# Performance work log

Hardware: AMD Instinct MI355X
Metric: run time of the kernel (lower is better)

Reference implementation:

```python
import jax, jax.numpy as jnp
import numpy as np

# Module hyperparameters (from init_kwargs)
CH = 512        # channels
H = 8           # num_heads
D = CH // H     # head_dim = 64
K = 64          # max_kernel_size
HALF_S = 16     # max_samples // 2
S = 2 * HALF_S + 1  # 33 sample taps
MAX_F = 16.0
MIN_F = 1.0
MAX_RECEPTIVE = HALF_S * MAX_F  # 256.0


def setup_inputs() -> dict:
    key = jax.random.key(0)
    ks = jax.random.split(key, 5)
    B, L = 2, 2048
    x = jax.random.normal(ks[0], (B, L, CH), dtype=jnp.float32)
    wave_w = jax.random.normal(ks[1], (2 * H, CH), dtype=jnp.float32) * 0.02
    wave_b = jnp.zeros((2 * H,), dtype=jnp.float32)
    kernel_w = jax.random.normal(ks[2], (H * K, CH), dtype=jnp.float32) * 0.02
    kernel_b = jnp.zeros((H * K,), dtype=jnp.float32)
    out_w = jax.random.normal(ks[3], (CH, CH), dtype=jnp.float32) * 0.02
    return {"x": x, "wave_w": wave_w, "wave_b": wave_b,
            "kernel_w": kernel_w, "kernel_b": kernel_b, "out_w": out_w}


def _silu(v):
    return v * jax.nn.sigmoid(v)


def _gather_conv(x, freq, phase, kernel):
    """Learned-frequency gather convolution.
    x:      [B,L,C]      freq,phase: [B,L,H]      kernel: [B,L,H,K]
    For each query position t and head h, sample S positions
      pos_j = t + phase + (j - half_s) * freq,   j = 0..S-1
    clamped to a receptive window of +-max_receptive around t and to [0,L-1],
    gathered with linear interpolation, weighted by per-position kernel taps.
    Phase receives no gradient (torch backward returns d_phase=None).
    """
    B, L, C = x.shape
    xh = x.reshape(B, L, H, D).transpose(0, 2, 1, 3)  # [B,H,L,D]
    t = jnp.arange(L, dtype=x.dtype)                  # [L]
    offs = jnp.arange(S, dtype=x.dtype) - HALF_S      # [S]
    phase_sg = jax.lax.stop_gradient(phase)
    tb = t[None, :, None, None]
    pos = tb + phase_sg[..., None] + offs * freq[..., None]   # [B,L,H,S]
    pos = jnp.clip(pos, tb - MAX_RECEPTIVE, tb + MAX_RECEPTIVE)
    pos = jnp.clip(pos, 0.0, L - 1)
    p0 = jnp.floor(pos)
    w = (pos - p0).transpose(0, 2, 1, 3)[..., None]           # [B,H,L,S,1]
    i0 = p0.astype(jnp.int32).transpose(0, 2, 1, 3).reshape(B, H, L * S)
    i1 = jnp.minimum(i0 + 1, L - 1)
    g0 = jnp.take_along_axis(xh, i0[..., None], axis=2).reshape(B, H, L, S, D)
    g1 = jnp.take_along_axis(xh, i1[..., None], axis=2).reshape(B, H, L, S, D)
    g = (1.0 - w) * g0 + w * g1                               # [B,H,L,S,D]
    k = kernel[..., :S].transpose(0, 2, 1, 3)                 # [B,H,L,S]
    outh = jnp.einsum('bhls,bhlsd->bhld', k, g)               # [B,H,L,D]
    return outh.transpose(0, 2, 1, 3).reshape(B, L, C)


def reference(x, wave_w, wave_b, kernel_w, kernel_b, out_w):
    B, L, C = x.shape
    wave = _silu(x @ wave_w.T + wave_b).reshape(B, L, 2, H)
    freq = jax.nn.sigmoid(wave[:, :, 0, :]) * (MAX_F - MIN_F) + MIN_F  # [B,L,H]
    phase = jnp.tanh(wave[:, :, 1, :]) * MAX_F                         # [B,L,H]
    kern = _silu(x @ kernel_w.T + kernel_b).reshape(B, L, H, K)
    hidden = _gather_conv(x, freq, phase, kern)                        # [B,L,C]
    return _silu(hidden @ out_w.T)
```

## Files before the change

### kernel.cpp

```cpp
#include <hip/hip_runtime.h>
#include <cstdint>
#include <cstddef>

#define LSEQ   2048
#define CHN    512
#define NH     8
#define HD     64
#define NTAP   33
#define NPOS   4096
#define MAXREC 256.0f

typedef __bf16   bf16x8 __attribute__((ext_vector_type(8)));
typedef __bf16   bf16x4 __attribute__((ext_vector_type(4)));
typedef float    f32x4  __attribute__((ext_vector_type(4)));
typedef _Float16 f16x2  __attribute__((ext_vector_type(2)));

__device__ __forceinline__ float silu_f(float v) {
    return v / (1.0f + expf(-v));
}

__device__ __forceinline__ void gload_lds16(const void* g, void* l) {
    __builtin_amdgcn_global_load_lds((const __attribute__((address_space(1))) void*)g,
                                     (__attribute__((address_space(3))) void*)l, 16, 0, 0);
}

__device__ __forceinline__ float fdot2f(unsigned a, unsigned b, float c) {
#if __has_builtin(__builtin_amdgcn_fdot2)
    return __builtin_amdgcn_fdot2(__builtin_bit_cast(f16x2, a),
                                  __builtin_bit_cast(f16x2, b), c, false);
#else
    f16x2 av = __builtin_bit_cast(f16x2, a);
    f16x2 bv = __builtin_bit_cast(f16x2, b);
    return c + (float)av[0] * (float)bv[0] + (float)av[1] * (float)bv[1];
#endif
}


__global__ __launch_bounds__(256) void fused_prep(
    const float* __restrict__ x, const float* __restrict__ ww,
    const float* __restrict__ wb,
    const float* __restrict__ kernel_w, __bf16* __restrict__ kwb,
    const float* __restrict__ out_w,    __bf16* __restrict__ owb,
    unsigned* __restrict__ tab, __bf16* __restrict__ xb,
    unsigned* __restrict__ xpair)
{
    __shared__ float wwS[16 * 512];
    __shared__ float fphS[4][16];

    int tid = threadIdx.x;
    if (blockIdx.x < 256) {
        const float* src = (blockIdx.x < 128) ? kernel_w : out_w;
        __bf16*      dst = (blockIdx.x < 128) ? kwb : owb;
        int C = ((blockIdx.x & 127) * 256 + tid);
        int tileIdx = C / (64 * 8);
        int o    = (C % (64 * 8)) * 16;
        int rowL = o >> 7;
        int cb   = o & 127;
        int cbu  = cb ^ ((rowL & 7) << 4);
        int block = cbu >> 6;
        int g2    = (cbu >> 4) & 3;
        int rs = (tileIdx >> 3) * 64 + rowL;
        int kb = (tileIdx & 7) * 64 + block * 32 + g2 * 4;
        const float* s = src + (size_t)rs * 512 + kb;
        float4 v0 = *(const float4*)s;
        float4 v1 = *(const float4*)(s + 16);
        bf16x8 r;
        r[0] = (__bf16)v0.x; r[1] = (__bf16)v0.y; r[2] = (__bf16)v0.z; r[3] = (__bf16)v0.w;
        r[4] = (__bf16)v1.x; r[5] = (__bf16)v1.y; r[6] = (__bf16)v1.z; r[7] = (__bf16)v1.w;
        *(bf16x8*)(dst + (size_t)C * 8) = r;
        return;
    }

    #pragma unroll
    for (int j = 0; j < 8; ++j) {
        int idx = tid * 4 + j * 1024;
        *(float4*)&wwS[idx] = *(const float4*)&ww[idx];
    }

    int wid  = tid >> 6;
    int lane = tid & 63;
    int pos  = (blockIdx.x - 256) * 4 + wid;
    int t    = pos & (LSEQ - 1);

    const float* xrow = x + (size_t)pos * CHN;
    float4 xa = *(const float4*)(xrow + lane * 8);
    float4 xv = *(const float4*)(xrow + lane * 8 + 4);
    int nxt = (t == LSEQ - 1) ? pos : pos + 1;
    const float* nrow = x + (size_t)nxt * CHN;
    float4 na = *(const float4*)(nrow + lane * 8);
    float4 nv = *(const float4*)(nrow + lane * 8 + 4);
    float xs[8];
    #pragma unroll
    for (int j = 0; j < 8; ++j) xs[j] = xrow[lane + 64 * j];

    {
        int kloc = (lane * 8) & 63;
        int kt   = lane >> 3;
        int rowL = pos & 63;
        int blk  = kloc >> 5;
        int kkA  = kloc & 31;
        int kkV  = kkA + 4;
        int colA = blk * 32 + 8 * ((kkA & 15) >> 2) + 4 * ((kkA >> 4) & 1);
        int colV = blk * 32 + 8 * ((kkV & 15) >> 2) + 4 * ((kkV >> 4) & 1);
        int sw   = (rowL & 7) << 4;
        char* base = (char*)xb + (((size_t)(pos >> 6) * 8 + kt) * 8192) + rowL * 128;
        bf16x4 va = { (__bf16)xa.x, (__bf16)xa.y, (__bf16)xa.z, (__bf16)xa.w };
        bf16x4 vv = { (__bf16)xv.x, (__bf16)xv.y, (__bf16)xv.z, (__bf16)xv.w };
        *(bf16x4*)(base + ((colA * 2) ^ sw)) = va;
        *(bf16x4*)(base + ((colV * 2) ^ sw)) = vv;
    }

    {
        float va8[8] = {xa.x, xa.y, xa.z, xa.w, xv.x, xv.y, xv.z, xv.w};
        float nb8[8] = {na.x, na.y, na.z, na.w, nv.x, nv.y, nv.z, nv.w};
        unsigned u[8];
        #pragma unroll
        for (int j = 0; j < 8; ++j) {
            unsigned short lo = __builtin_bit_cast(unsigned short, (_Float16)va8[j]);
            unsigned short hi = __builtin_bit_cast(unsigned short, (_Float16)nb8[j]);
            u[j] = (unsigned)lo | ((unsigned)hi << 16);
        }
        unsigned* dp = xpair + (size_t)pos * 512 + lane * 8;
        *(uint4*)dp       = make_uint4(u[0], u[1], u[2], u[3]);
        *(uint4*)(dp + 4) = make_uint4(u[4], u[5], u[6], u[7]);
    }

    __syncthreads();

    #pragma unroll
    for (int o = 0; o < 16; ++o) {
        const float* wr = &wwS[o * 512 + lane];
        float p = 0.0f;
        #pragma unroll
        for (int j = 0; j < 8; ++j) p = fmaf(xs[j], wr[64 * j], p);
        #pragma unroll
        for (int off = 32; off > 0; off >>= 1) p += __shfl_xor(p, off);
        if (lane == 0) {
            float v = p + wb[o];
            float s = silu_f(v);
            fphS[wid][o] = (o < 8) ? (1.0f + 15.0f / (1.0f + expf(-s)))
                                   : (tanhf(s) * 16.0f);
        }
    }
    __syncthreads();

    float tf = (float)t;
    float lo = fmaxf(tf - MAXREC, 0.0f);
    float hi = fminf(tf + MAXREC, (float)(LSEQ - 1));
    for (int it = lane; it < NH * NTAP; it += 64) {
        int h = it & 7, s = it >> 3;
        float f  = fphS[wid][h];
        float ph = fphS[wid][8 + h];
        float p = (tf + ph) + (float)(s - 16) * f;
        p = fminf(fmaxf(p, lo), hi);
        float p0 = floorf(p);
        float w  = p - p0;
        int i0 = (int)p0;
        if (i0 >= LSEQ - 1) { i0 = LSEQ - 2; w = 1.0f; }
        _Float16 hw = (_Float16)w;
        unsigned u = ((unsigned)i0 << 16) |
                     (unsigned)__builtin_bit_cast(unsigned short, hw);
        tab[(size_t)pos * (NH * NTAP) + it] = u;
    }
}

template<bool COMPACT>
__global__ __launch_bounds__(256) void gemm_mfma64(
    const __bf16* __restrict__ At, const __bf16* __restrict__ Bt,
    const float* __restrict__ bias, float* __restrict__ C,
    uint2* __restrict__ qtab, const unsigned* __restrict__ tab)
{
    __shared__ __bf16 As[2][64 * 64];
    __shared__ __bf16 Bs[2][64 * 64];

    int bm = blockIdx.x, bn = blockIdx.y;
    int tid  = threadIdx.x;
    int lane = tid & 63;
    int wid  = tid >> 6;
    int wr = wid >> 1, wc = wid & 1;
    int lg = lane >> 4, l15 = lane & 15;

    const __bf16* Abase = At + (size_t)bm * 8 * 4096;
    const __bf16* Bbase = Bt + (size_t)bn * 8 * 4096;

    int offA[2][2], offB[2][2];
    #pragma unroll
    for (int mi = 0; mi < 2; ++mi) {
        int row = wr * 32 + mi * 16 + l15;
        #pragma unroll
        for (int ks = 0; ks < 2; ++ks)
            offA[mi][ks] = row * 128 + (((ks << 6) | (lg << 4)) ^ ((row & 7) << 4));
    }
    #pragma unroll
    for (int ni = 0; ni < 2; ++ni) {
        int n = wc * 32 + ni * 16 + l15;
        #pragma unroll
        for (int ks = 0; ks < 2; ++ks)
            offB[ni][ks] = n * 128 + (((ks << 6) | (lg << 4)) ^ ((n & 7) << 4));
    }

    f32x4 acc[2][2] = {};

    auto stage = [&](int b, int kt) {
        const __bf16* ga = Abase + (size_t)kt * 4096 + tid * 8;
        const __bf16* gb = Bbase + (size_t)kt * 4096 + tid * 8;
        __bf16* la = &As[b][tid * 8];
        __bf16* lb = &Bs[b][tid * 8];
        #pragma unroll
        for (int c = 0; c < 2; ++c) gload_lds16(ga + c * 2048, la + c * 2048);
        #pragma unroll
        for (int c = 0; c < 2; ++c) gload_lds16(gb + c * 2048, lb + c * 2048);
    };

    stage(0, 0);
    #pragma unroll
    for (int kt = 0; kt < 8; ++kt) {
        int cur = kt & 1;
        if (kt < 7) stage(cur ^ 1, kt + 1);
        __builtin_amdgcn_sched_barrier(0);
        if (kt < 7) asm volatile("s_waitcnt vmcnt(4)" ::: "memory");
        else        asm volatile("s_waitcnt vmcnt(0)" ::: "memory");
        __builtin_amdgcn_s_barrier();
        const char* ab = (const char*)&As[cur][0];
        const char* bb = (const char*)&Bs[cur][0];
        #pragma unroll
        for (int ks = 0; ks < 2; ++ks) {
            bf16x8 af[2], bfr[2];
            #pragma unroll
            for (int mi = 0; mi < 2; ++mi) af[mi]  = *(const bf16x8*)(ab + offA[mi][ks]);
            #pragma unroll
            for (int ni = 0; ni < 2; ++ni) bfr[ni] = *(const bf16x8*)(bb + offB[ni][ks]);
            #pragma unroll
            for (int mi = 0; mi < 2; ++mi)
                #pragma unroll
                for (int ni = 0; ni < 2; ++ni)
                    acc[mi][ni] = __builtin_amdgcn_mfma_f32_16x16x32_bf16(
                        af[mi], bfr[ni], acc[mi][ni], 0, 0, 0);
        }
        __builtin_amdgcn_s_barrier();
    }

    int n0 = bn * 64 + wc * 32 + l15;
    #pragma unroll
    for (int ni = 0; ni < 2; ++ni) {
        int n = n0 + ni * 16;
        float bv = bias ? bias[n] : 0.0f;
        #pragma unroll
        for (int mi = 0; mi < 2; ++mi) {
            int m = bm * 64 + wr * 32 + mi * 16 + lg * 4;
            #pragma unroll
            for (int j = 0; j < 4; ++j) {
                float v = silu_f(acc[mi][ni][j] + bv);
                if (COMPACT) {
                    int h = n >> 6, sc = n & 63;
                    if (sc < NTAP) {
                        unsigned u = tab[(size_t)(m + j) * (NH * NTAP) + sc * 8 + h];
                        float w = (float)__builtin_bit_cast(
                            _Float16, (unsigned short)(u & 0xFFFFu));
                        float t1 = v * w;
                        unsigned short c0 =
                            __builtin_bit_cast(unsigned short, (_Float16)(v - t1));
                        unsigned short c1 =
                            __builtin_bit_cast(unsigned short, (_Float16)t1);
                        uint2 qv;
                        qv.x = (unsigned)c0 | ((unsigned)c1 << 16);
                        qv.y = (u >> 16) << 11;
                        qtab[(size_t)(m + j) * (NTAP * 8) + sc * 8 + h] = qv;
                    }
                } else {
                    C[(size_t)(m + j) * 512 + n] = v;
                }
            }
        }
    }
}

__global__ __launch_bounds__(256, 4) void gather_conv(
    const unsigned* __restrict__ xpair, const uint2* __restrict__ qtab,
    __bf16* __restrict__ hb)
{
    __shared__ uint2 qs[4][NTAP + 3];

    int wid  = threadIdx.x >> 6;
    int lane = threadIdx.x & 63;
    int bid  = blockIdx.x;
    int nb   = ((bid & 7) << 9) | (bid >> 3);
    int wix  = nb * 4 + wid;
    int h = wix & 7, t = wix >> 3;
    int b = blockIdx.y;

    int pos = b * LSEQ + t;
    const char* xpb = (const char*)xpair + (size_t)b * (LSEQ * 2048);
    int xoff = (h * HD + lane) * 4;
    const uint2* qp = qtab + (size_t)pos * (NTAP * 8) + h;

    if (lane < NTAP) qs[wid][lane] = qp[lane * 8];
    __syncthreads();

    float acc = 0.0f;
    #pragma unroll
    for (int c = 0; c < 3; ++c) {
        unsigned cx[11];
        unsigned gv[11];
        #pragma unroll
        for (int i = 0; i < 11; ++i) {
            uint2 q = qs[wid][c * 11 + i];
            cx[i] = q.x;
            unsigned off = __builtin_amdgcn_readfirstlane(q.y);
            gv[i] = *(const unsigned*)(xpb + off + xoff);
        }
        #pragma unroll
        for (int i = 0; i < 11; ++i) acc = fdot2f(cx[i], gv[i], acc);
    }

    int tile = (pos >> 6) * 8 + h;
    int rowL = pos & 63;
    int d = lane, blk = d >> 5, kk = d & 31;
    int colp = blk * 32 + (kk & 3) + (((kk >> 4) & 1) << 2) + (((kk & 15) >> 2) << 3);
    int byteS = (colp * 2) ^ ((rowL & 7) << 4);
    hb[(size_t)tile * 4096 + rowL * 64 + (byteS >> 1)] = (__bf16)acc;
}

extern "C" void kernel_launch(void* const* d_in, const int* in_sizes, int n_in,
                              void* d_out, int out_size, void* d_ws, size_t ws_size,
                              hipStream_t stream)
{
    const float* x        = (const float*)d_in[0];
    const float* wave_w   = (const float*)d_in[1];
    const float* wave_b   = (const float*)d_in[2];
    const float* kernel_w = (const float*)d_in[3];
    const float* kernel_b = (const float*)d_in[4];
    const float* out_w    = (const float*)d_in[5];
    float* out = (float*)d_out;

    char* ws = (char*)d_ws;
    unsigned* tab   = (unsigned*)ws;  ws += (size_t)NPOS * NH * NTAP * 4;
    uint2*    qtab  = (uint2*)ws;     ws += (size_t)NPOS * NH * NTAP * 8;
    unsigned* xpair = (unsigned*)ws;  ws += (size_t)NPOS * CHN * 4;
    __bf16*   xb    = (__bf16*)ws;    ws += (size_t)NPOS * CHN * 2;
    __bf16*   kwb   = (__bf16*)ws;    ws += (size_t)CHN * CHN * 2;
    __bf16*   owb   = (__bf16*)ws;    ws += (size_t)CHN * CHN * 2;
    __bf16*   hidb  = xb;

    fused_prep<<<256 + NPOS / 4, 256, 0, stream>>>(
        x, wave_w, wave_b, kernel_w, kwb, out_w, owb, tab, xb, xpair);

    dim3 gg(NPOS / 64, CHN / 64);
    gemm_mfma64<true><<<gg, 256, 0, stream>>>(xb, kwb, kernel_b, nullptr, qtab, tab);

    gather_conv<<<dim3(LSEQ * NH / 4, 2), 256, 0, stream>>>(xpair, qtab, hidb);

    gemm_mfma64<false><<<gg, 256, 0, stream>>>(hidb, owb, nullptr, out, nullptr, nullptr);
}
```

Before: 55.59 us.

## Load GEMM B tiles straight into registers and batch all gather taps

```diff
diff --git a/kernel.cpp b/kernel.cpp
--- a/kernel.cpp
+++ b/kernel.cpp
@@ -171,7 +171,6 @@
     uint2* __restrict__ qtab, const unsigned* __restrict__ tab)
 {
     __shared__ __bf16 As[2][64 * 64];
-    __shared__ __bf16 Bs[2][64 * 64];
 
     int bm = blockIdx.x, bn = blockIdx.y;
     int tid  = threadIdx.x;
@@ -181,7 +180,7 @@
     int lg = lane >> 4, l15 = lane & 15;
 
     const __bf16* Abase = At + (size_t)bm * 8 * 4096;
-    const __bf16* Bbase = Bt + (size_t)bn * 8 * 4096;
+    const char*   Bbase = (const char*)(Bt + (size_t)bn * 8 * 4096);
 
     int offA[2][2], offB[2][2];
     #pragma unroll
@@ -200,42 +199,50 @@
     }
 
     f32x4 acc[2][2] = {};
-
-    auto stage = [&](int b, int kt) {
+    bf16x8 breg[2][2][2];
+
+    auto stageA = [&](int b, int kt) {
         const __bf16* ga = Abase + (size_t)kt * 4096 + tid * 8;
-        const __bf16* gb = Bbase + (size_t)kt * 4096 + tid * 8;
         __bf16* la = &As[b][tid * 8];
-        __bf16* lb = &Bs[b][tid * 8];
         #pragma unroll
         for (int c = 0; c < 2; ++c) gload_lds16(ga + c * 2048, la + c * 2048);
-        #pragma unroll
-        for (int c = 0; c < 2; ++c) gload_lds16(gb + c * 2048, lb + c * 2048);
     };
 
-    stage(0, 0);
+    stageA(0, 0);
+    #pragma unroll
+    for (int ni = 0; ni < 2; ++ni)
+        #pragma unroll
+        for (int ks = 0; ks < 2; ++ks)
+            breg[0][ni][ks] = *(const bf16x8*)(Bbase + offB[ni][ks]);
+
     #pragma unroll
     for (int kt = 0; kt < 8; ++kt) {
         int cur = kt & 1;
-        if (kt < 7) stage(cur ^ 1, kt + 1);
+        if (kt < 7) {
+            stageA(cur ^ 1, kt + 1);
+            #pragma unroll
+            for (int ni = 0; ni < 2; ++ni)
+                #pragma unroll
+                for (int ks = 0; ks < 2; ++ks)
+                    breg[cur ^ 1][ni][ks] =
+                        *(const bf16x8*)(Bbase + (size_t)(kt + 1) * 8192 + offB[ni][ks]);
+        }
         __builtin_amdgcn_sched_barrier(0);
-        if (kt < 7) asm volatile("s_waitcnt vmcnt(4)" ::: "memory");
+        if (kt < 7) asm volatile("s_waitcnt vmcnt(6)" ::: "memory");
         else        asm volatile("s_waitcnt vmcnt(0)" ::: "memory");
         __builtin_amdgcn_s_barrier();
         const char* ab = (const char*)&As[cur][0];
-        const char* bb = (const char*)&Bs[cur][0];
         #pragma unroll
         for (int ks = 0; ks < 2; ++ks) {
-            bf16x8 af[2], bfr[2];
+            bf16x8 af[2];
             #pragma unroll
-            for (int mi = 0; mi < 2; ++mi) af[mi]  = *(const bf16x8*)(ab + offA[mi][ks]);
-            #pragma unroll
-            for (int ni = 0; ni < 2; ++ni) bfr[ni] = *(const bf16x8*)(bb + offB[ni][ks]);
+            for (int mi = 0; mi < 2; ++mi) af[mi] = *(const bf16x8*)(ab + offA[mi][ks]);
             #pragma unroll
             for (int mi = 0; mi < 2; ++mi)
                 #pragma unroll
                 for (int ni = 0; ni < 2; ++ni)
                     acc[mi][ni] = __builtin_amdgcn_mfma_f32_16x16x32_bf16(
-                        af[mi], bfr[ni], acc[mi][ni], 0, 0, 0);
+                        af[mi], breg[cur][ni][ks], acc[mi][ni], 0, 0, 0);
         }
         __builtin_amdgcn_s_barrier();
     }
@@ -295,23 +302,21 @@
     const uint2* qp = qtab + (size_t)pos * (NTAP * 8) + h;
 
     if (lane < NTAP) qs[wid][lane] = qp[lane * 8];
-    __syncthreads();
-
+    asm volatile("s_waitcnt lgkmcnt(0)" ::: "memory");
+    __builtin_amdgcn_sched_barrier(0);
+
+    unsigned cx[NTAP];
+    unsigned gv[NTAP];
+    #pragma unroll
+    for (int i = 0; i < NTAP; ++i) {
+        uint2 q = qs[wid][i];
+        cx[i] = q.x;
+        unsigned off = __builtin_amdgcn_readfirstlane(q.y);
+        gv[i] = *(const unsigned*)(xpb + off + xoff);
+    }
     float acc = 0.0f;
     #pragma unroll
-    for (int c = 0; c < 3; ++c) {
-        unsigned cx[11];
-        unsigned gv[11];
-        #pragma unroll
-        for (int i = 0; i < 11; ++i) {
-            uint2 q = qs[wid][c * 11 + i];
-            cx[i] = q.x;
-            unsigned off = __builtin_amdgcn_readfirstlane(q.y);
-            gv[i] = *(const unsigned*)(xpb + off + xoff);
-        }
-        #pragma unroll
-        for (int i = 0; i < 11; ++i) acc = fdot2f(cx[i], gv[i], acc);
-    }
+    for (int i = 0; i < NTAP; ++i) acc = fdot2f(cx[i], gv[i], acc);
 
     int tile = (pos >> 6) * 8 + h;
     int rowL = pos & 63;
```

Result: slower. 65.40 us (+17.6%).

## Fuse kernel-tap GEMM with gather convolution via shared-memory tap table

Applied to the files above, without the earlier changes.

```diff
diff --git a/kernel.cpp b/kernel.cpp
--- a/kernel.cpp
+++ b/kernel.cpp
@@ -164,11 +164,162 @@
     }
 }
 
-template<bool COMPACT>
+__global__ __launch_bounds__(256) void gemm1_gather(
+    const __bf16* __restrict__ At, const __bf16* __restrict__ Bt,
+    const float* __restrict__ bias, const unsigned* __restrict__ tab,
+    const unsigned* __restrict__ xpair, __bf16* __restrict__ hb)
+{
+    __shared__ __align__(16) char smem[32768];
+    __bf16* As0 = (__bf16*)smem;
+    __bf16* Bs0 = (__bf16*)(smem + 16384);
+    uint2*  qsL = (uint2*)smem;
+
+    int lb = blockIdx.x;
+    int bm = (lb & 7) * 8 + ((lb >> 3) & 7);
+    int h  = lb >> 6;
+
+    int tid  = threadIdx.x;
+    int lane = tid & 63;
+    int wid  = tid >> 6;
+    int wr = wid >> 1, wc = wid & 1;
+    int lg = lane >> 4, l15 = lane & 15;
+
+    const __bf16* Abase = At + (size_t)bm * 8 * 4096;
+    const __bf16* Bbase = Bt + (size_t)h * 8 * 4096;
+
+    int offA[2][2], offB[2][2];
+    #pragma unroll
+    for (int mi = 0; mi < 2; ++mi) {
+        int row = wr * 32 + mi * 16 + l15;
+        #pragma unroll
+        for (int ks = 0; ks < 2; ++ks)
+            offA[mi][ks] = row * 128 + (((ks << 6) | (lg << 4)) ^ ((row & 7) << 4));
+    }
+    #pragma unroll
+    for (int ni = 0; ni < 2; ++ni) {
+        int n = wc * 32 + ni * 16 + l15;
+        #pragma unroll
+        for (int ks = 0; ks < 2; ++ks)
+            offB[ni][ks] = n * 128 + (((ks << 6) | (lg << 4)) ^ ((n & 7) << 4));
+    }
+
+    f32x4 acc[2][2] = {};
+
+    auto stage = [&](int b, int kt) {
+        const __bf16* ga = Abase + (size_t)kt * 4096 + tid * 8;
+        const __bf16* gb = Bbase + (size_t)kt * 4096 + tid * 8;
+        __bf16* la = As0 + b * 4096 + tid * 8;
+        __bf16* lb_ = Bs0 + b * 4096 + tid * 8;
+        #pragma unroll
+        for (int c = 0; c < 2; ++c) gload_lds16(ga + c * 2048, la + c * 2048);
+        #pragma unroll
+        for (int c = 0; c < 2; ++c) gload_lds16(gb + c * 2048, lb_ + c * 2048);
+    };
+
+    stage(0, 0);
+    #pragma unroll
+    for (int kt = 0; kt < 8; ++kt) {
+        int cur = kt & 1;
+        if (kt < 7) stage(cur ^ 1, kt + 1);
+        __builtin_amdgcn_sched_barrier(0);
+        if (kt < 7) asm volatile("s_waitcnt vmcnt(4)" ::: "memory");
+        else        asm volatile("s_waitcnt vmcnt(0)" ::: "memory");
+        __builtin_amdgcn_s_barrier();
+        const char* ab = (const char*)(As0 + cur * 4096);
+        const char* bb = (const char*)(Bs0 + cur * 4096);
+        #pragma unroll
+        for (int ks = 0; ks < 2; ++ks) {
+            bf16x8 af[2], bfr[2];
+            #pragma unroll
+            for (int mi = 0; mi < 2; ++mi) af[mi]  = *(const bf16x8*)(ab + offA[mi][ks]);
+            #pragma unroll
+            for (int ni = 0; ni < 2; ++ni) bfr[ni] = *(const bf16x8*)(bb + offB[ni][ks]);
+            #pragma unroll
+            for (int mi = 0; mi < 2; ++mi)
+                #pragma unroll
+                for (int ni = 0; ni < 2; ++ni)
+                    acc[mi][ni] = __builtin_amdgcn_mfma_f32_16x16x32_bf16(
+                        af[mi], bfr[ni], acc[mi][ni], 0, 0, 0);
+        }
+        __builtin_amdgcn_s_barrier();
+    }
+
+    #pragma unroll
+    for (int ni = 0; ni < 2; ++ni) {
+        int n = wc * 32 + ni * 16 + l15;
+        float bv = bias[h * 64 + n];
+        #pragma unroll
+        for (int mi = 0; mi < 2; ++mi) {
+            int ml = wr * 32 + mi * 16 + lg * 4;
+            #pragma unroll
+            for (int j = 0; j < 4; ++j) {
+                if (n < NTAP) {
+                    float v = silu_f(acc[mi][ni][j] + bv);
+                    int m = bm * 64 + ml + j;
+                    unsigned u = tab[(size_t)m * (NH * NTAP) + n * 8 + h];
+                    float w = (float)__builtin_bit_cast(
+                        _Float16, (unsigned short)(u & 0xFFFFu));
+                    float t1 = v * w;
+                    unsigned short c0 =
+                        __builtin_bit_cast(unsigned short, (_Float16)(v - t1));
+                    unsigned short c1 =
+                        __builtin_bit_cast(unsigned short, (_Float16)t1);
+                    uint2 qv;
+                    qv.x = (unsigned)c0 | ((unsigned)c1 << 16);
+                    qv.y = ((unsigned)(m & ~(LSEQ - 1)) + (u >> 16)) << 11;
+                    qsL[(ml + j) * NTAP + n] = qv;
+                }
+            }
+        }
+    }
+    __syncthreads();
+
+    int xoff = (h * HD + lane) * 4;
+    const char* xpb = (const char*)xpair;
+    #pragma unroll 1
+    for (int p = 0; p < 16; ++p) {
+        int ml = wid * 16 + p;
+        int pos = bm * 64 + ml;
+        const uint2* qr = &qsL[ml * NTAP];
+
+        float acc2 = 0.0f;
+        {
+            unsigned cx[17], gv[17];
+            #pragma unroll
+            for (int i = 0; i < 17; ++i) {
+                uint2 q = qr[i];
+                cx[i] = q.x;
+                unsigned off = __builtin_amdgcn_readfirstlane(q.y);
+                gv[i] = *(const unsigned*)(xpb + off + xoff);
+            }
+            #pragma unroll
+            for (int i = 0; i < 17; ++i) acc2 = fdot2f(cx[i], gv[i], acc2);
+        }
+        {
+            unsigned cx[16], gv[16];
+            #pragma unroll
+            for (int i = 0; i < 16; ++i) {
+                uint2 q = qr[17 + i];
+                cx[i] = q.x;
+                unsigned off = __builtin_amdgcn_readfirstlane(q.y);
+                gv[i] = *(const unsigned*)(xpb + off + xoff);
+            }
+            #pragma unroll
+            for (int i = 0; i < 16; ++i) acc2 = fdot2f(cx[i], gv[i], acc2);
+        }
+
+        int tile = bm * 8 + h;
+        int rowL = ml;
+        int d = lane, blk = d >> 5, kk = d & 31;
+        int colp = blk * 32 + (kk & 3) + (((kk >> 4) & 1) << 2) + (((kk & 15) >> 2) << 3);
+        int byteS = (colp * 2) ^ ((rowL & 7) << 4);
+        hb[(size_t)tile * 4096 + rowL * 64 + (byteS >> 1)] = (__bf16)acc2;
+    }
+}
+
 __global__ __launch_bounds__(256) void gemm_mfma64(
     const __bf16* __restrict__ At, const __bf16* __restrict__ Bt,
-    const float* __restrict__ bias, float* __restrict__ C,
-    uint2* __restrict__ qtab, const unsigned* __restrict__ tab)
+    float* __restrict__ C)
 {
     __shared__ __bf16 As[2][64 * 64];
     __shared__ __bf16 Bs[2][64 * 64];
@@ -244,81 +395,14 @@
     #pragma unroll
     for (int ni = 0; ni < 2; ++ni) {
         int n = n0 + ni * 16;
-        float bv = bias ? bias[n] : 0.0f;
         #pragma unroll
         for (int mi = 0; mi < 2; ++mi) {
             int m = bm * 64 + wr * 32 + mi * 16 + lg * 4;
             #pragma unroll
-            for (int j = 0; j < 4; ++j) {
-                float v = silu_f(acc[mi][ni][j] + bv);
-                if (COMPACT) {
-                    int h = n >> 6, sc = n & 63;
-                    if (sc < NTAP) {
-                        unsigned u = tab[(size_t)(m + j) * (NH * NTAP) + sc * 8 + h];
-                        float w = (float)__builtin_bit_cast(
-                            _Float16, (unsigned short)(u & 0xFFFFu));
-                        float t1 = v * w;
-                        unsigned short c0 =
-                            __builtin_bit_cast(unsigned short, (_Float16)(v - t1));
-                        unsigned short c1 =
-                            __builtin_bit_cast(unsigned short, (_Float16)t1);
-                        uint2 qv;
-                        qv.x = (unsigned)c0 | ((unsigned)c1 << 16);
-                        qv.y = (u >> 16) << 11;
-                        qtab[(size_t)(m + j) * (NTAP * 8) + sc * 8 + h] = qv;
-                    }
-                } else {
-                    C[(size_t)(m + j) * 512 + n] = v;
-                }
-            }
-        }
-    }
-}
-
-__global__ __launch_bounds__(256, 4) void gather_conv(
-    const unsigned* __restrict__ xpair, const uint2* __restrict__ qtab,
-    __bf16* __restrict__ hb)
-{
-    __shared__ uint2 qs[4][NTAP + 3];
-
-    int wid  = threadIdx.x >> 6;
-    int lane = threadIdx.x & 63;
-    int bid  = blockIdx.x;
-    int nb   = ((bid & 7) << 9) | (bid >> 3);
-    int wix  = nb * 4 + wid;
-    int h = wix & 7, t = wix >> 3;
-    int b = blockIdx.y;
-
-    int pos = b * LSEQ + t;
-    const char* xpb = (const char*)xpair + (size_t)b * (LSEQ * 2048);
-    int xoff = (h * HD + lane) * 4;
-    const uint2* qp = qtab + (size_t)pos * (NTAP * 8) + h;
-
-    if (lane < NTAP) qs[wid][lane] = qp[lane * 8];
-    __syncthreads();
-
-    float acc = 0.0f;
-    #pragma unroll
-    for (int c = 0; c < 3; ++c) {
-        unsigned cx[11];
-        unsigned gv[11];
-        #pragma unroll
-        for (int i = 0; i < 11; ++i) {
-            uint2 q = qs[wid][c * 11 + i];
-            cx[i] = q.x;
-            unsigned off = __builtin_amdgcn_readfirstlane(q.y);
-            gv[i] = *(const unsigned*)(xpb + off + xoff);
-        }
-        #pragma unroll
-        for (int i = 0; i < 11; ++i) acc = fdot2f(cx[i], gv[i], acc);
-    }
-
-    int tile = (pos >> 6) * 8 + h;
-    int rowL = pos & 63;
-    int d = lane, blk = d >> 5, kk = d & 31;
-    int colp = blk * 32 + (kk & 3) + (((kk >> 4) & 1) << 2) + (((kk & 15) >> 2) << 3);
-    int byteS = (colp * 2) ^ ((rowL & 7) << 4);
-    hb[(size_t)tile * 4096 + rowL * 64 + (byteS >> 1)] = (__bf16)acc;
+            for (int j = 0; j < 4; ++j)
+                C[(size_t)(m + j) * 512 + n] = silu_f(acc[mi][ni][j]);
+        }
+    }
 }
 
 extern "C" void kernel_launch(void* const* d_in, const int* in_sizes, int n_in,
@@ -335,20 +419,16 @@
 
     char* ws = (char*)d_ws;
     unsigned* tab   = (unsigned*)ws;  ws += (size_t)NPOS * NH * NTAP * 4;
-    uint2*    qtab  = (uint2*)ws;     ws += (size_t)NPOS * NH * NTAP * 8;
     unsigned* xpair = (unsigned*)ws;  ws += (size_t)NPOS * CHN * 4;
     __bf16*   xb    = (__bf16*)ws;    ws += (size_t)NPOS * CHN * 2;
+    __bf16*   hidb  = (__bf16*)ws;    ws += (size_t)NPOS * CHN * 2;
     __bf16*   kwb   = (__bf16*)ws;    ws += (size_t)CHN * CHN * 2;
     __bf16*   owb   = (__bf16*)ws;    ws += (size_t)CHN * CHN * 2;
-    __bf16*   hidb  = xb;
 
     fused_prep<<<256 + NPOS / 4, 256, 0, stream>>>(
         x, wave_w, wave_b, kernel_w, kwb, out_w, owb, tab, xb, xpair);
 
-    dim3 gg(NPOS / 64, CHN / 64);
-    gemm_mfma64<true><<<gg, 256, 0, stream>>>(xb, kwb, kernel_b, nullptr, qtab, tab);
-
-    gather_conv<<<dim3(LSEQ * NH / 4, 2), 256, 0, stream>>>(xpair, qtab, hidb);
-
-    gemm_mfma64<false><<<gg, 256, 0, stream>>>(hidb, owb, nullptr, out, nullptr, nullptr);
-}
+    gemm1_gather<<<512, 256, 0, stream>>>(xb, kwb, kernel_b, tab, xpair, hidb);
+
+    gemm_mfma64<<<dim3(NPOS / 64, CHN / 64), 256, 0, stream>>>(hidb, owb, out);
+}
```

Measured after the change: 64.11 us. 1.15x slower.

## Loop four positions per prep block and issue all gather taps at once

Applied to the files above, without the earlier changes.

```diff
diff --git a/kernel.cpp b/kernel.cpp
--- a/kernel.cpp
+++ b/kernel.cpp
@@ -76,91 +76,94 @@
         int idx = tid * 4 + j * 1024;
         *(float4*)&wwS[idx] = *(const float4*)&ww[idx];
     }
+    __syncthreads();
 
     int wid  = tid >> 6;
     int lane = tid & 63;
-    int pos  = (blockIdx.x - 256) * 4 + wid;
-    int t    = pos & (LSEQ - 1);
-
-    const float* xrow = x + (size_t)pos * CHN;
-    float4 xa = *(const float4*)(xrow + lane * 8);
-    float4 xv = *(const float4*)(xrow + lane * 8 + 4);
-    int nxt = (t == LSEQ - 1) ? pos : pos + 1;
-    const float* nrow = x + (size_t)nxt * CHN;
-    float4 na = *(const float4*)(nrow + lane * 8);
-    float4 nv = *(const float4*)(nrow + lane * 8 + 4);
-    float xs[8];
-    #pragma unroll
-    for (int j = 0; j < 8; ++j) xs[j] = xrow[lane + 64 * j];
-
-    {
-        int kloc = (lane * 8) & 63;
-        int kt   = lane >> 3;
-        int rowL = pos & 63;
-        int blk  = kloc >> 5;
-        int kkA  = kloc & 31;
-        int kkV  = kkA + 4;
-        int colA = blk * 32 + 8 * ((kkA & 15) >> 2) + 4 * ((kkA >> 4) & 1);
-        int colV = blk * 32 + 8 * ((kkV & 15) >> 2) + 4 * ((kkV >> 4) & 1);
-        int sw   = (rowL & 7) << 4;
-        char* base = (char*)xb + (((size_t)(pos >> 6) * 8 + kt) * 8192) + rowL * 128;
-        bf16x4 va = { (__bf16)xa.x, (__bf16)xa.y, (__bf16)xa.z, (__bf16)xa.w };
-        bf16x4 vv = { (__bf16)xv.x, (__bf16)xv.y, (__bf16)xv.z, (__bf16)xv.w };
-        *(bf16x4*)(base + ((colA * 2) ^ sw)) = va;
-        *(bf16x4*)(base + ((colV * 2) ^ sw)) = vv;
-    }
-
-    {
-        float va8[8] = {xa.x, xa.y, xa.z, xa.w, xv.x, xv.y, xv.z, xv.w};
-        float nb8[8] = {na.x, na.y, na.z, na.w, nv.x, nv.y, nv.z, nv.w};
-        unsigned u[8];
-        #pragma unroll
-        for (int j = 0; j < 8; ++j) {
-            unsigned short lo = __builtin_bit_cast(unsigned short, (_Float16)va8[j]);
-            unsigned short hi = __builtin_bit_cast(unsigned short, (_Float16)nb8[j]);
-            u[j] = (unsigned)lo | ((unsigned)hi << 16);
-        }
-        unsigned* dp = xpair + (size_t)pos * 512 + lane * 8;
-        *(uint4*)dp       = make_uint4(u[0], u[1], u[2], u[3]);
-        *(uint4*)(dp + 4) = make_uint4(u[4], u[5], u[6], u[7]);
-    }
-
-    __syncthreads();
-
-    #pragma unroll
-    for (int o = 0; o < 16; ++o) {
-        const float* wr = &wwS[o * 512 + lane];
-        float p = 0.0f;
-        #pragma unroll
-        for (int j = 0; j < 8; ++j) p = fmaf(xs[j], wr[64 * j], p);
-        #pragma unroll
-        for (int off = 32; off > 0; off >>= 1) p += __shfl_xor(p, off);
-        if (lane == 0) {
-            float v = p + wb[o];
-            float s = silu_f(v);
-            fphS[wid][o] = (o < 8) ? (1.0f + 15.0f / (1.0f + expf(-s)))
-                                   : (tanhf(s) * 16.0f);
-        }
-    }
-    __syncthreads();
-
-    float tf = (float)t;
-    float lo = fmaxf(tf - MAXREC, 0.0f);
-    float hi = fminf(tf + MAXREC, (float)(LSEQ - 1));
-    for (int it = lane; it < NH * NTAP; it += 64) {
-        int h = it & 7, s = it >> 3;
-        float f  = fphS[wid][h];
-        float ph = fphS[wid][8 + h];
-        float p = (tf + ph) + (float)(s - 16) * f;
-        p = fminf(fmaxf(p, lo), hi);
-        float p0 = floorf(p);
-        float w  = p - p0;
-        int i0 = (int)p0;
-        if (i0 >= LSEQ - 1) { i0 = LSEQ - 2; w = 1.0f; }
-        _Float16 hw = (_Float16)w;
-        unsigned u = ((unsigned)i0 << 16) |
-                     (unsigned)__builtin_bit_cast(unsigned short, hw);
-        tab[(size_t)pos * (NH * NTAP) + it] = u;
+    int base = (blockIdx.x - 256) * 16;
+
+    #pragma unroll 1
+    for (int it = 0; it < 4; ++it) {
+        int pos = base + it * 4 + wid;
+        int t   = pos & (LSEQ - 1);
+
+        const float* xrow = x + (size_t)pos * CHN;
+        float4 xa = *(const float4*)(xrow + lane * 8);
+        float4 xv = *(const float4*)(xrow + lane * 8 + 4);
+        int nxt = (t == LSEQ - 1) ? pos : pos + 1;
+        const float* nrow = x + (size_t)nxt * CHN;
+        float4 na = *(const float4*)(nrow + lane * 8);
+        float4 nv = *(const float4*)(nrow + lane * 8 + 4);
+        float xs[8];
+        #pragma unroll
+        for (int j = 0; j < 8; ++j) xs[j] = xrow[lane + 64 * j];
+
+        {
+            int kloc = (lane * 8) & 63;
+            int kt   = lane >> 3;
+            int rowL = pos & 63;
+            int blk  = kloc >> 5;
+            int kkA  = kloc & 31;
+            int kkV  = kkA + 4;
+            int colA = blk * 32 + 8 * ((kkA & 15) >> 2) + 4 * ((kkA >> 4) & 1);
+            int colV = blk * 32 + 8 * ((kkV & 15) >> 2) + 4 * ((kkV >> 4) & 1);
+            int sw   = (rowL & 7) << 4;
+            char* bp = (char*)xb + (((size_t)(pos >> 6) * 8 + kt) * 8192) + rowL * 128;
+            bf16x4 va = { (__bf16)xa.x, (__bf16)xa.y, (__bf16)xa.z, (__bf16)xa.w };
+            bf16x4 vv = { (__bf16)xv.x, (__bf16)xv.y, (__bf16)xv.z, (__bf16)xv.w };
+            *(bf16x4*)(bp + ((colA * 2) ^ sw)) = va;
+            *(bf16x4*)(bp + ((colV * 2) ^ sw)) = vv;
+        }
+
+        {
+            float va8[8] = {xa.x, xa.y, xa.z, xa.w, xv.x, xv.y, xv.z, xv.w};
+            float nb8[8] = {na.x, na.y, na.z, na.w, nv.x, nv.y, nv.z, nv.w};
+            unsigned u[8];
+            #pragma unroll
+            for (int j = 0; j < 8; ++j) {
+                unsigned short lo = __builtin_bit_cast(unsigned short, (_Float16)va8[j]);
+                unsigned short hi = __builtin_bit_cast(unsigned short, (_Float16)nb8[j]);
+                u[j] = (unsigned)lo | ((unsigned)hi << 16);
+            }
+            unsigned* dp = xpair + (size_t)pos * 512 + lane * 8;
+            *(uint4*)dp       = make_uint4(u[0], u[1], u[2], u[3]);
+            *(uint4*)(dp + 4) = make_uint4(u[4], u[5], u[6], u[7]);
+        }
+
+        #pragma unroll
+        for (int o = 0; o < 16; ++o) {
+            const float* wr = &wwS[o * 512 + lane];
+            float p = 0.0f;
+            #pragma unroll
+            for (int j = 0; j < 8; ++j) p = fmaf(xs[j], wr[64 * j], p);
+            #pragma unroll
+            for (int off = 32; off > 0; off >>= 1) p += __shfl_xor(p, off);
+            if (lane == 0) {
+                float v = p + wb[o];
+                float s = silu_f(v);
+                fphS[wid][o] = (o < 8) ? (1.0f + 15.0f / (1.0f + expf(-s)))
+                                       : (tanhf(s) * 16.0f);
+            }
+        }
+
+        float tf = (float)t;
+        float lo = fmaxf(tf - MAXREC, 0.0f);
+        float hi = fminf(tf + MAXREC, (float)(LSEQ - 1));
+        for (int itap = lane; itap < NH * NTAP; itap += 64) {
+            int h = itap & 7, s = itap >> 3;
+            float f  = fphS[wid][h];
+            float ph = fphS[wid][8 + h];
+            float p = (tf + ph) + (float)(s - 16) * f;
+            p = fminf(fmaxf(p, lo), hi);
+            float p0 = floorf(p);
+            float w  = p - p0;
+            int i0 = (int)p0;
+            if (i0 >= LSEQ - 1) { i0 = LSEQ - 2; w = 1.0f; }
+            _Float16 hw = (_Float16)w;
+            unsigned u = ((unsigned)i0 << 16) |
+                         (unsigned)__builtin_bit_cast(unsigned short, hw);
+            tab[(size_t)pos * (NH * NTAP) + itap] = u;
+        }
     }
 }
 
@@ -295,23 +298,21 @@
     const uint2* qp = qtab + (size_t)pos * (NTAP * 8) + h;
 
     if (lane < NTAP) qs[wid][lane] = qp[lane * 8];
-    __syncthreads();
-
+    asm volatile("s_waitcnt lgkmcnt(0)" ::: "memory");
+    __builtin_amdgcn_sched_barrier(0);
+
+    unsigned cx[NTAP];
+    unsigned gv[NTAP];
+    #pragma unroll
+    for (int i = 0; i < NTAP; ++i) {
+        uint2 q = qs[wid][i];
+        cx[i] = q.x;
+        unsigned off = __builtin_amdgcn_readfirstlane(q.y);
+        gv[i] = *(const unsigned*)(xpb + off + xoff);
+    }
     float acc = 0.0f;
     #pragma unroll
-    for (int c = 0; c < 3; ++c) {
-        unsigned cx[11];
-        unsigned gv[11];
-        #pragma unroll
-        for (int i = 0; i < 11; ++i) {
-            uint2 q = qs[wid][c * 11 + i];
-            cx[i] = q.x;
-            unsigned off = __builtin_amdgcn_readfirstlane(q.y);
-            gv[i] = *(const unsigned*)(xpb + off + xoff);
-        }
-        #pragma unroll
-        for (int i = 0; i < 11; ++i) acc = fdot2f(cx[i], gv[i], acc);
-    }
+    for (int i = 0; i < NTAP; ++i) acc = fdot2f(cx[i], gv[i], acc);
 
     int tile = (pos >> 6) * 8 + h;
     int rowL = pos & 63;
@@ -342,7 +343,7 @@
     __bf16*   owb   = (__bf16*)ws;    ws += (size_t)CHN * CHN * 2;
     __bf16*   hidb  = xb;
 
-    fused_prep<<<256 + NPOS / 4, 256, 0, stream>>>(
+    fused_prep<<<512, 256, 0, stream>>>(
         x, wave_w, wave_b, kernel_w, kwb, out_w, owb, tab, xb, xpair);
 
     dim3 gg(NPOS / 64, CHN / 64);
```

New measurement: 79.18 us. 42.4% more time.
